# Kernel optimization log

Measured on AMD Instinct MI355X. Metric: run time of the kernel, lower is better.

The kernel has to match this reference:

```python
import jax, jax.numpy as jnp
import numpy as np

N = 50000
E = 1000000
FN = 16
FE = 8
H = 64
DH = 64
LN_EPS = 1e-5


def _layernorm(x, g, b):
    mu = jnp.mean(x, axis=-1, keepdims=True)
    var = jnp.var(x, axis=-1, keepdims=True)
    return (x - mu) * jax.lax.rsqrt(var + LN_EPS) * g + b


def setup_inputs() -> dict:
    key = jax.random.key(0)
    ks = jax.random.split(key, 24)

    def w(k, i, o):
        return jax.random.normal(k, (i, o), jnp.float32) / np.sqrt(i).astype(np.float32)

    inp = {}
    inp["x"] = jax.random.normal(ks[0], (N, FN), jnp.float32)
    inp["edge_index"] = jax.random.randint(ks[1], (2, E), 0, N, dtype=jnp.int32)
    inp["edge_attr"] = jax.random.normal(ks[2], (E, FE), jnp.float32)
    # layer 0 (in_dim = FN, residual is a Linear since FN != H)
    inp["l0_lin_w"] = w(ks[3], FE, FN); inp["l0_lin_b"] = jnp.zeros((FN,), jnp.float32)
    inp["l0_w1"] = w(ks[4], FN, H);    inp["l0_b1"] = jnp.zeros((H,), jnp.float32)
    inp["l0_w2"] = w(ks[5], H, H);     inp["l0_b2"] = jnp.zeros((H,), jnp.float32)
    inp["l0_ln_g"] = jnp.ones((H,), jnp.float32); inp["l0_ln_b"] = jnp.zeros((H,), jnp.float32)
    inp["l0_res_w"] = w(ks[6], FN, H); inp["l0_res_b"] = jnp.zeros((H,), jnp.float32)
    # layers 1, 2 (in_dim = H, residual = identity)
    for li, base in ((1, 7), (2, 11)):
        inp[f"l{li}_lin_w"] = w(ks[base], FE, H);   inp[f"l{li}_lin_b"] = jnp.zeros((H,), jnp.float32)
        inp[f"l{li}_w1"] = w(ks[base + 1], H, H);   inp[f"l{li}_b1"] = jnp.zeros((H,), jnp.float32)
        inp[f"l{li}_w2"] = w(ks[base + 2], H, H);   inp[f"l{li}_b2"] = jnp.zeros((H,), jnp.float32)
        inp[f"l{li}_ln_g"] = jnp.ones((H,), jnp.float32)
        inp[f"l{li}_ln_b"] = jnp.zeros((H,), jnp.float32)
    D_IN = 4 * H + FE
    inp["dec_w1"] = w(ks[20], D_IN, DH);    inp["dec_b1"] = jnp.zeros((DH,), jnp.float32)
    inp["dec_w2"] = w(ks[21], DH, DH // 2); inp["dec_b2"] = jnp.zeros((DH // 2,), jnp.float32)
    inp["dec_w3"] = w(ks[22], DH // 2, 1);  inp["dec_b3"] = jnp.zeros((1,), jnp.float32)
    return inp


def _block(x, src, dst, edge_attr, lin_w, lin_b, w1, b1, w2, b2, ln_g, ln_b, res):
    # GINEConv: message = ReLU(x_src + Lin(edge_attr)); sum-aggregate at dst; eps=0
    msg = jax.nn.relu(x[src] + edge_attr @ lin_w + lin_b)      # (E, D_in)
    aggr = jax.ops.segment_sum(msg, dst, num_segments=N)       # (N, D_in)
    h = jax.nn.relu((x + aggr) @ w1 + b1) @ w2 + b2            # GIN nn MLP -> (N, H)
    h = jax.nn.relu(h)                                         # dropout inactive (eval)
    return _layernorm(h + res, ln_g, ln_b)


def reference(x, edge_index, edge_attr,
              l0_lin_w, l0_lin_b, l0_w1, l0_b1, l0_w2, l0_b2, l0_ln_g, l0_ln_b, l0_res_w, l0_res_b,
              l1_lin_w, l1_lin_b, l1_w1, l1_b1, l1_w2, l1_b2, l1_ln_g, l1_ln_b,
              l2_lin_w, l2_lin_b, l2_w1, l2_b1, l2_w2, l2_b2, l2_ln_g, l2_ln_b,
              dec_w1, dec_b1, dec_w2, dec_b2, dec_w3, dec_b3):
    src, dst = edge_index[0], edge_index[1]
    h = _block(x, src, dst, edge_attr, l0_lin_w, l0_lin_b, l0_w1, l0_b1, l0_w2, l0_b2,
               l0_ln_g, l0_ln_b, x @ l0_res_w + l0_res_b)
    h = _block(h, src, dst, edge_attr, l1_lin_w, l1_lin_b, l1_w1, l1_b1, l1_w2, l1_b2,
               l1_ln_g, l1_ln_b, h)
    h = _block(h, src, dst, edge_attr, l2_lin_w, l2_lin_b, l2_w1, l2_b1, l2_w2, l2_b2,
               l2_ln_g, l2_ln_b, h)
    hs, hd = h[src], h[dst]                                    # (E, H) each
    z = jnp.concatenate([hs, hd, jnp.abs(hs - hd), hs * hd, edge_attr], axis=-1)  # (E, 4H+FE)
    z = jax.nn.relu(z @ dec_w1 + dec_b1)
    z = jax.nn.relu(z @ dec_w2 + dec_b2)
    return (z @ dec_w3 + dec_b3)[:, 0]                         # (E,)
```

## Files before the change

### kernel.cpp

```cpp
#include <hip/hip_runtime.h>

#define NN 50000
#define NE 1000000

constexpr float LN_EPS = 1e-5f;

typedef short bf16x8 __attribute__((ext_vector_type(8)));
typedef float f32x4 __attribute__((ext_vector_type(4)));
typedef uint uvec4 __attribute__((ext_vector_type(4)));
typedef uint uvec2 __attribute__((ext_vector_type(2)));

__device__ inline uint cvtpk(float a, float b) {
  uint r;
  asm("v_cvt_pk_bf16_f32 %0, %1, %2" : "=v"(r) : "v"(a), "v"(b));
  return r;
}
__device__ inline ushort cvt1(float a) {
  uint r;
  asm("v_cvt_pk_bf16_f32 %0, %1, %1" : "=v"(r) : "v"(a));
  return (ushort)r;
}
__device__ inline float bflo(uint u) { union { uint x; float f; } v; v.x = u << 16; return v.f; }
__device__ inline float bfhi(uint u) { union { uint x; float f; } v; v.x = u & 0xffff0000u; return v.f; }

__global__ __launch_bounds__(256) void hist_kernel(const int* __restrict__ ei,
                                                   int* __restrict__ cnt) {
  int e = blockIdx.x * 256 + threadIdx.x;
  if (e < NE) atomicAdd(&cnt[ei[NE + e]], 1);
}

__global__ __launch_bounds__(256) void scan1_kernel(const int* __restrict__ cnt,
                                                    int* __restrict__ off,
                                                    int* __restrict__ bsum) {
  __shared__ int sh[256];
  int t = threadIdx.x;
  int idx = blockIdx.x * 256 + t;
  int v = (idx < NN) ? cnt[idx] : 0;
  sh[t] = v;
  __syncthreads();
  for (int o = 1; o < 256; o <<= 1) {
    int xv = (t >= o) ? sh[t - o] : 0;
    __syncthreads();
    sh[t] += xv;
    __syncthreads();
  }
  if (idx <= NN) off[idx] = sh[t] - v;
  if (t == 255) bsum[blockIdx.x] = sh[255];
}

__global__ __launch_bounds__(256) void scan2_kernel(int* __restrict__ bsum, int nb) {
  __shared__ int sh[256];
  int t = threadIdx.x;
  int v = (t < nb) ? bsum[t] : 0;
  sh[t] = v;
  __syncthreads();
  for (int o = 1; o < 256; o <<= 1) {
    int xv = (t >= o) ? sh[t - o] : 0;
    __syncthreads();
    sh[t] += xv;
    __syncthreads();
  }
  if (t < nb) bsum[t] = sh[t] - v;
}

__global__ __launch_bounds__(256) void scan3_kernel(int* __restrict__ off,
                                                    const int* __restrict__ bsum,
                                                    int* __restrict__ cnt) {
  int idx = blockIdx.x * 256 + threadIdx.x;
  if (idx <= NN) off[idx] += bsum[blockIdx.x];
  if (idx < NN) cnt[idx] = 0;
}

__global__ __launch_bounds__(256) void scatter_kernel(
    const int* __restrict__ ei, const float* __restrict__ ea,
    const int* __restrict__ off, int* __restrict__ cur,
    int* __restrict__ ipos, int* __restrict__ srcp, int* __restrict__ dstp,
    ushort* __restrict__ eapb) {
  int e = blockIdx.x * 256 + threadIdx.x;
  if (e < NE) {
    int d = ei[NE + e];
    int s = ei[e];
    int p = off[d] + atomicAdd(&cur[d], 1);
    ipos[e] = p;
    srcp[p] = s;
    dstp[p] = d;
    const float* eaf = ea + (size_t)e * 8;
    f32x4 e0 = *(const f32x4*)(eaf);
    f32x4 e1 = *(const f32x4*)(eaf + 4);
    uvec4 u;
    u.x = cvtpk(e0.x, e0.y);
    u.y = cvtpk(e0.z, e0.w);
    u.z = cvtpk(e1.x, e1.y);
    u.w = cvtpk(e1.z, e1.w);
    __builtin_nontemporal_store(u, (uvec4*)(eapb + (size_t)p * 8));
  }
}

__global__ __launch_bounds__(256) void unperm_kernel(const float* __restrict__ tmp,
                                                     const int* __restrict__ ipos,
                                                     float* __restrict__ out) {
  int e = blockIdx.x * 256 + threadIdx.x;
  if (e < NE) out[e] = tmp[ipos[e]];
}

__global__ __launch_bounds__(256) void aggr0_kernel(
    const float* __restrict__ x, float* __restrict__ tout16,
    const ushort* __restrict__ eapb, const int* __restrict__ srcp,
    const int* __restrict__ off,
    const float* __restrict__ lw, const float* __restrict__ lb) {
  int n = blockIdx.x * 4 + (threadIdx.x >> 6);
  int j = threadIdx.x & 63;
  int d = j & 15, slot = j >> 4;
  int start = off[n], end = off[n + 1];
  float lwv[8];
#pragma unroll
  for (int i = 0; i < 8; i++) lwv[i] = lw[i * 16 + d];
  float lbv = lb[d];
  float acc = 0.f;
  for (int base = start; base < end; base += 64) {
    int idx = base + j;
    int sl = (idx < end) ? srcp[idx] : 0;
    int c = min(end - base, 64);
    for (int i0 = 0; i0 < c; i0 += 4) {
      int i = i0 + slot;
      bool valid = i < c;
      int ii = i & 63;
      int s = __shfl(sl, ii);
      int pp = min(base + i0 + slot, NE - 1);
      float ev = bflo((uint)eapb[(size_t)pp * 8 + (d & 7)]);
      float xs = x[(size_t)s * 16 + d];
      float m = lbv + xs;
#pragma unroll
      for (int q = 0; q < 8; q++) m = fmaf(__shfl(ev, slot * 16 + q), lwv[q], m);
      m = fmaxf(m, 0.f);
      acc += valid ? m : 0.f;
    }
  }
  acc += __shfl_xor(acc, 16);
  acc += __shfl_xor(acc, 32);
  if (slot == 0) tout16[(size_t)n * 16 + d] = acc;
}

__device__ inline float edge8_msg(const ushort* __restrict__ hinb, int s, int j,
                                  uint ulo, uint uhi, uint vlo, uint vhi,
                                  const float* lwv, float lbv) {
  float hc = bflo((uint)hinb[(size_t)s * 64 + j]);
  float m = lbv + hc;
  m = fmaf(bflo(ulo), lwv[0], m);
  m = fmaf(bfhi(ulo), lwv[1], m);
  m = fmaf(bflo(uhi), lwv[2], m);
  m = fmaf(bfhi(uhi), lwv[3], m);
  m = fmaf(bflo(vlo), lwv[4], m);
  m = fmaf(bfhi(vlo), lwv[5], m);
  m = fmaf(bflo(vhi), lwv[6], m);
  m = fmaf(bfhi(vhi), lwv[7], m);
  return fmaxf(m, 0.f);
}

__global__ __launch_bounds__(256) void aggr_kernel(
    const ushort* __restrict__ hinb, float* __restrict__ tout,
    const ushort* __restrict__ eapb, const int* __restrict__ srcp,
    const int* __restrict__ off,
    const float* __restrict__ lw, const float* __restrict__ lb) {
  int n = blockIdx.x * 4 + (threadIdx.x >> 6);
  int j = threadIdx.x & 63;
  int start = __builtin_amdgcn_readfirstlane(off[n]);
  int end = __builtin_amdgcn_readfirstlane(off[n + 1]);
  float lwv[8];
#pragma unroll
  for (int i = 0; i < 8; i++) lwv[i] = lw[i * 64 + j];
  float lbv = lb[j];
  float acc = 0.f;
  int p = start;
  for (; p + 8 <= end; p += 8) {
    const uvec4* ip = (const uvec4*)(srcp + p);
    uvec4 I0 = __builtin_nontemporal_load(ip + 0);
    uvec4 I1 = __builtin_nontemporal_load(ip + 1);
    int s0 = __builtin_amdgcn_readfirstlane((int)I0.x);
    int s1 = __builtin_amdgcn_readfirstlane((int)I0.y);
    int s2 = __builtin_amdgcn_readfirstlane((int)I0.z);
    int s3 = __builtin_amdgcn_readfirstlane((int)I0.w);
    int s4 = __builtin_amdgcn_readfirstlane((int)I1.x);
    int s5 = __builtin_amdgcn_readfirstlane((int)I1.y);
    int s6 = __builtin_amdgcn_readfirstlane((int)I1.z);
    int s7 = __builtin_amdgcn_readfirstlane((int)I1.w);
    const uvec4* ep = (const uvec4*)(eapb + (size_t)p * 8);
    uint ua[8][4];
#pragma unroll
    for (int i = 0; i < 8; i++) {
      uvec4 E = __builtin_nontemporal_load(ep + i);
      ua[i][0] = __builtin_amdgcn_readfirstlane(E.x);
      ua[i][1] = __builtin_amdgcn_readfirstlane(E.y);
      ua[i][2] = __builtin_amdgcn_readfirstlane(E.z);
      ua[i][3] = __builtin_amdgcn_readfirstlane(E.w);
    }
    acc += edge8_msg(hinb, s0, j, ua[0][0], ua[0][1], ua[0][2], ua[0][3], lwv, lbv);
    acc += edge8_msg(hinb, s1, j, ua[1][0], ua[1][1], ua[1][2], ua[1][3], lwv, lbv);
    acc += edge8_msg(hinb, s2, j, ua[2][0], ua[2][1], ua[2][2], ua[2][3], lwv, lbv);
    acc += edge8_msg(hinb, s3, j, ua[3][0], ua[3][1], ua[3][2], ua[3][3], lwv, lbv);
    acc += edge8_msg(hinb, s4, j, ua[4][0], ua[4][1], ua[4][2], ua[4][3], lwv, lbv);
    acc += edge8_msg(hinb, s5, j, ua[5][0], ua[5][1], ua[5][2], ua[5][3], lwv, lbv);
    acc += edge8_msg(hinb, s6, j, ua[6][0], ua[6][1], ua[6][2], ua[6][3], lwv, lbv);
    acc += edge8_msg(hinb, s7, j, ua[7][0], ua[7][1], ua[7][2], ua[7][3], lwv, lbv);
  }
  for (; p < end; p++) {
    int s = __builtin_amdgcn_readfirstlane(srcp[p]);
    uvec4 E = __builtin_nontemporal_load((const uvec4*)(eapb + (size_t)p * 8));
    uint e0 = __builtin_amdgcn_readfirstlane(E.x);
    uint e1 = __builtin_amdgcn_readfirstlane(E.y);
    uint e2 = __builtin_amdgcn_readfirstlane(E.z);
    uint e3 = __builtin_amdgcn_readfirstlane(E.w);
    acc += edge8_msg(hinb, s, j, e0, e1, e2, e3, lwv, lbv);
  }
  tout[(size_t)n * 64 + j] = acc;
}

__global__ __launch_bounds__(256) void prep_kernel(
    const float* __restrict__ w1, const float* __restrict__ w2,
    ushort* __restrict__ w1f, ushort* __restrict__ w2f) {
  int t = blockIdx.x * 256 + threadIdx.x;
  if (t < 18432) {
    int j = t & 7, lane = (t >> 3) & 63, f = t >> 9;
    int k = (f >> 2) * 32 + ((lane >> 4) * 8) + j;
    int n = (f & 3) * 16 + (lane & 15);
    float v = (k < 264) ? w1[k * 64 + n] : 0.f;
    w1f[t] = cvt1(v);
  } else {
    int t2 = t - 18432;
    int j = t2 & 7, lane = (t2 >> 3) & 63, f = t2 >> 9;
    int k = (f >> 1) * 32 + ((lane >> 4) * 8) + j;
    int n = (f & 1) * 16 + (lane & 15);
    w2f[t2] = cvt1(w2[k * 32 + n]);
  }
}

__global__ __launch_bounds__(256) void prep_mlpw(
    const float* __restrict__ w1a, const float* __restrict__ w2a,
    const float* __restrict__ w1b, const float* __restrict__ w2b,
    ushort* __restrict__ out) {
  int t = blockIdx.x * 256 + threadIdx.x;
  int layer = t >> 13, wsel = (t >> 12) & 1, idx = t & 4095;
  const float* w = layer ? (wsel ? w2b : w1b) : (wsel ? w2a : w1a);
  int j = idx & 7, lane = (idx >> 3) & 63, f = idx >> 9;
  int k = (f >> 2) * 32 + ((lane >> 4) * 8) + j;
  int n = (f & 3) * 16 + (lane & 15);
  float v = w[k * 64 + n];
  ushort h = cvt1(v);
  float r = v - bflo((uint)h);
  ushort lo = cvt1(r);
  int base = layer * 16384 + wsel * 8192;
  out[base + idx] = h;
  out[base + 4096 + idx] = lo;
}

__global__ __launch_bounds__(256) void prep_mlp0(
    const float* __restrict__ w1, const float* __restrict__ w2,
    const float* __restrict__ rw, ushort* __restrict__ out) {
  int t = blockIdx.x * 256 + threadIdx.x;
  if (t < 4096) {
    int which = t >> 11, idx = t & 2047;
    int j = idx & 7, lane = (idx >> 3) & 63, f = idx >> 9;
    int k = ((lane >> 4) * 8) + j;
    int n = f * 16 + (lane & 15);
    float v;
    if (which == 0) v = (k < 16) ? w1[k * 64 + n] : 0.f;
    else            v = (k >= 16) ? rw[(k - 16) * 64 + n] : 0.f;
    ushort h = cvt1(v);
    float r = v - bflo((uint)h);
    int base = which * 4096;
    out[base + idx] = h;
    out[base + 2048 + idx] = cvt1(r);
  } else {
    int idx = t - 4096;
    int j = idx & 7, lane = (idx >> 3) & 63, f = idx >> 9;
    int k = (f >> 2) * 32 + ((lane >> 4) * 8) + j;
    int n = (f & 3) * 16 + (lane & 15);
    float v = w2[k * 64 + n];
    ushort h = cvt1(v);
    float r = v - bflo((uint)h);
    out[8192 + idx] = h;
    out[12288 + idx] = cvt1(r);
  }
}

#define YS2 68

__global__ __launch_bounds__(128) void mlp_kernel(
    const float* __restrict__ tacc, const float* __restrict__ hinf,
    float* __restrict__ houtf, ushort* __restrict__ houtbf,
    const ushort* __restrict__ wf,
    const float* __restrict__ b1, const float* __restrict__ b2,
    const float* __restrict__ lng, const float* __restrict__ lnb) {
  __shared__ float ybuf[2][32 * YS2];
  const int w = threadIdx.x >> 6, l = threadIdx.x & 63;
  const int sub = l & 15, quad = l >> 4;
  const int wid = blockIdx.x * 2 + w;
  const int r0 = wid * 32;
  if (r0 >= NN) return;
  float* Y = ybuf[w];

  const bf16x8* w1h = (const bf16x8*)wf;
  const bf16x8* w1l = (const bf16x8*)(wf + 4096);
  const bf16x8* w2h = (const bf16x8*)(wf + 8192);
  const bf16x8* w2l = (const bf16x8*)(wf + 12288);

  union UF { uvec4 u; bf16x8 v; };

  bf16x8 Ahi[2][2], Alo[2][2];
#pragma unroll
  for (int m = 0; m < 2; m++) {
    int row = min(r0 + m * 16 + sub, NN - 1);
    const float* pt = tacc + (size_t)row * 64 + quad * 8;
    const float* ph = hinf + (size_t)row * 64 + quad * 8;
#pragma unroll
    for (int ks = 0; ks < 2; ks++) {
      f32x4 t0 = *(const f32x4*)(pt + ks * 32);
      f32x4 t1 = *(const f32x4*)(pt + ks * 32 + 4);
      f32x4 h0 = *(const f32x4*)(ph + ks * 32);
      f32x4 h1 = *(const f32x4*)(ph + ks * 32 + 4);
      t0 += h0;
      t1 += h1;
      UF uh, ul;
      uh.u.x = cvtpk(t0.x, t0.y);
      uh.u.y = cvtpk(t0.z, t0.w);
      uh.u.z = cvtpk(t1.x, t1.y);
      uh.u.w = cvtpk(t1.z, t1.w);
      ul.u.x = cvtpk(t0.x - bflo(uh.u.x), t0.y - bfhi(uh.u.x));
      ul.u.y = cvtpk(t0.z - bflo(uh.u.y), t0.w - bfhi(uh.u.y));
      ul.u.z = cvtpk(t1.x - bflo(uh.u.z), t1.y - bfhi(uh.u.z));
      ul.u.w = cvtpk(t1.z - bflo(uh.u.w), t1.w - bfhi(uh.u.w));
      Ahi[m][ks] = uh.v;
      Alo[m][ks] = ul.v;
    }
  }

  f32x4 c1[2][4];
#pragma unroll
  for (int m = 0; m < 2; m++)
#pragma unroll
    for (int nb = 0; nb < 4; nb++) c1[m][nb] = (f32x4){0.f, 0.f, 0.f, 0.f};
#pragma unroll
  for (int nb = 0; nb < 4; nb++) {
#pragma unroll
    for (int ks = 0; ks < 2; ks++) {
      bf16x8 bh = w1h[(ks * 4 + nb) * 64 + l];
      bf16x8 bl = w1l[(ks * 4 + nb) * 64 + l];
      c1[0][nb] = __builtin_amdgcn_mfma_f32_16x16x32_bf16(Ahi[0][ks], bh, c1[0][nb], 0, 0, 0);
      c1[1][nb] = __builtin_amdgcn_mfma_f32_16x16x32_bf16(Ahi[1][ks], bh, c1[1][nb], 0, 0, 0);
      c1[0][nb] = __builtin_amdgcn_mfma_f32_16x16x32_bf16(Alo[0][ks], bh, c1[0][nb], 0, 0, 0);
      c1[1][nb] = __builtin_amdgcn_mfma_f32_16x16x32_bf16(Alo[1][ks], bh, c1[1][nb], 0, 0, 0);
      c1[0][nb] = __builtin_amdgcn_mfma_f32_16x16x32_bf16(Ahi[0][ks], bl, c1[0][nb], 0, 0, 0);
      c1[1][nb] = __builtin_amdgcn_mfma_f32_16x16x32_bf16(Ahi[1][ks], bl, c1[1][nb], 0, 0, 0);
    }
  }

  float b1v[4];
#pragma unroll
  for (int nb = 0; nb < 4; nb++) b1v[nb] = b1[nb * 16 + sub];
#pragma unroll
  for (int m = 0; m < 2; m++)
#pragma unroll
    for (int nb = 0; nb < 4; nb++)
#pragma unroll
      for (int r = 0; r < 4; r++)
        Y[(m * 16 + quad * 4 + r) * YS2 + nb * 16 + sub] =
            fmaxf(c1[m][nb][r] + b1v[nb], 0.f);

  bf16x8 Qhi[2][2], Qlo[2][2];
#pragma unroll
  for (int m = 0; m < 2; m++) {
#pragma unroll
    for (int ks = 0; ks < 2; ks++) {
      const float* py = &Y[(m * 16 + sub) * YS2 + ks * 32 + quad * 8];
      f32x4 q0 = *(const f32x4*)py;
      f32x4 q1 = *(const f32x4*)(py + 4);
      UF uh, ul;
      uh.u.x = cvtpk(q0.x, q0.y);
      uh.u.y = cvtpk(q0.z, q0.w);
      uh.u.z = cvtpk(q1.x, q1.y);
      uh.u.w = cvtpk(q1.z, q1.w);
      ul.u.x = cvtpk(q0.x - bflo(uh.u.x), q0.y - bfhi(uh.u.x));
      ul.u.y = cvtpk(q0.z - bflo(uh.u.y), q0.w - bfhi(uh.u.y));
      ul.u.z = cvtpk(q1.x - bflo(uh.u.z), q1.y - bfhi(uh.u.z));
      ul.u.w = cvtpk(q1.z - bflo(uh.u.w), q1.w - bfhi(uh.u.w));
      Qhi[m][ks] = uh.v;
      Qlo[m][ks] = ul.v;
    }
  }

  f32x4 c2[2][4];
#pragma unroll
  for (int m = 0; m < 2; m++)
#pragma unroll
    for (int nb = 0; nb < 4; nb++) c2[m][nb] = (f32x4){0.f, 0.f, 0.f, 0.f};
#pragma unroll
  for (int nb = 0; nb < 4; nb++) {
#pragma unroll
    for (int ks = 0; ks < 2; ks++) {
      bf16x8 bh = w2h[(ks * 4 + nb) * 64 + l];
      bf16x8 bl = w2l[(ks * 4 + nb) * 64 + l];
      c2[0][nb] = __builtin_amdgcn_mfma_f32_16x16x32_bf16(Qhi[0][ks], bh, c2[0][nb], 0, 0, 0);
      c2[1][nb] = __builtin_amdgcn_mfma_f32_16x16x32_bf16(Qhi[1][ks], bh, c2[1][nb], 0, 0, 0);
      c2[0][nb] = __builtin_amdgcn_mfma_f32_16x16x32_bf16(Qlo[0][ks], bh, c2[0][nb], 0, 0, 0);
      c2[1][nb] = __builtin_amdgcn_mfma_f32_16x16x32_bf16(Qlo[1][ks], bh, c2[1][nb], 0, 0, 0);
      c2[0][nb] = __builtin_amdgcn_mfma_f32_16x16x32_bf16(Qhi[0][ks], bl, c2[0][nb], 0, 0, 0);
      c2[1][nb] = __builtin_amdgcn_mfma_f32_16x16x32_bf16(Qhi[1][ks], bl, c2[1][nb], 0, 0, 0);
    }
  }

  float b2v[4], lngv[4], lnbv[4];
#pragma unroll
  for (int nb = 0; nb < 4; nb++) {
    b2v[nb] = b2[nb * 16 + sub];
    lngv[nb] = lng[nb * 16 + sub];
    lnbv[nb] = lnb[nb * 16 + sub];
  }
#pragma unroll
  for (int m = 0; m < 2; m++) {
#pragma unroll
    for (int r = 0; r < 4; r++) {
      int node = r0 + m * 16 + quad * 4 + r;
      int nc = min(node, NN - 1);
      float vp[4];
      float s = 0.f;
#pragma unroll
      for (int nb = 0; nb < 4; nb++) {
        vp[nb] = fmaxf(c2[m][nb][r] + b2v[nb], 0.f) +
                 hinf[(size_t)nc * 64 + nb * 16 + sub];
        s += vp[nb];
      }
      s += __shfl_xor(s, 1);
      s += __shfl_xor(s, 2);
      s += __shfl_xor(s, 4);
      s += __shfl_xor(s, 8);
      float mu = s * (1.f / 64.f);
      float vv = 0.f;
      float dv[4];
#pragma unroll
      for (int nb = 0; nb < 4; nb++) {
        dv[nb] = vp[nb] - mu;
        vv += dv[nb] * dv[nb];
      }
      vv += __shfl_xor(vv, 1);
      vv += __shfl_xor(vv, 2);
      vv += __shfl_xor(vv, 4);
      vv += __shfl_xor(vv, 8);
      float rstd = rsqrtf(vv * (1.f / 64.f) + LN_EPS);
      if (node < NN) {
#pragma unroll
        for (int nb = 0; nb < 4; nb++) {
          float o = dv[nb] * rstd * lngv[nb] + lnbv[nb];
          if (houtf) houtf[(size_t)node * 64 + nb * 16 + sub] = o;
          houtbf[(size_t)node * 64 + nb * 16 + sub] = cvt1(o);
        }
      }
    }
  }
}

__global__ __launch_bounds__(128) void mlp0_kernel(
    const float* __restrict__ x, const float* __restrict__ tacc16,
    float* __restrict__ houtf, ushort* __restrict__ houtbf,
    const ushort* __restrict__ wf,
    const float* __restrict__ b1, const float* __restrict__ b2,
    const float* __restrict__ rb,
    const float* __restrict__ lng, const float* __restrict__ lnb) {
  __shared__ float ybuf[2][32 * YS2];
  const int w = threadIdx.x >> 6, l = threadIdx.x & 63;
  const int sub = l & 15, quad = l >> 4;
  const int wid = blockIdx.x * 2 + w;
  const int r0 = wid * 32;
  if (r0 >= NN) return;
  float* Y = ybuf[w];

  const bf16x8* B1h = (const bf16x8*)wf;
  const bf16x8* B1l = (const bf16x8*)(wf + 2048);
  const bf16x8* B2h = (const bf16x8*)(wf + 4096);
  const bf16x8* B2l = (const bf16x8*)(wf + 6144);
  const bf16x8* W2h = (const bf16x8*)(wf + 8192);
  const bf16x8* W2l = (const bf16x8*)(wf + 12288);

  union UF { uvec4 u; bf16x8 v; };

  bf16x8 Ahi[2], Alo[2];
#pragma unroll
  for (int m = 0; m < 2; m++) {
    int row = min(r0 + m * 16 + sub, NN - 1);
    const float* px = x + (size_t)row * 16 + (quad & 1) * 8;
    f32x4 v0 = *(const f32x4*)px;
    f32x4 v1 = *(const f32x4*)(px + 4);
    if (quad < 2) {
      const float* pt = tacc16 + (size_t)row * 16 + (quad & 1) * 8;
      v0 += *(const f32x4*)pt;
      v1 += *(const f32x4*)(pt + 4);
    }
    UF uh, ul;
    uh.u.x = cvtpk(v0.x, v0.y);
    uh.u.y = cvtpk(v0.z, v0.w);
    uh.u.z = cvtpk(v1.x, v1.y);
    uh.u.w = cvtpk(v1.z, v1.w);
    ul.u.x = cvtpk(v0.x - bflo(uh.u.x), v0.y - bfhi(uh.u.x));
    ul.u.y = cvtpk(v0.z - bflo(uh.u.y), v0.w - bfhi(uh.u.y));
    ul.u.z = cvtpk(v1.x - bflo(uh.u.z), v1.y - bfhi(uh.u.z));
    ul.u.w = cvtpk(v1.z - bflo(uh.u.w), v1.w - bfhi(uh.u.w));
    Ahi[m] = uh.v;
    Alo[m] = ul.v;
  }

  f32x4 c1[2][4], cr[2][4];
#pragma unroll
  for (int m = 0; m < 2; m++)
#pragma unroll
    for (int nb = 0; nb < 4; nb++) {
      c1[m][nb] = (f32x4){0.f, 0.f, 0.f, 0.f};
      cr[m][nb] = (f32x4){0.f, 0.f, 0.f, 0.f};
    }
#pragma unroll
  for (int nb = 0; nb < 4; nb++) {
    bf16x8 bh = B1h[nb * 64 + l];
    bf16x8 bl = B1l[nb * 64 + l];
    c1[0][nb] = __builtin_amdgcn_mfma_f32_16x16x32_bf16(Ahi[0], bh, c1[0][nb], 0, 0, 0);
    c1[1][nb] = __builtin_amdgcn_mfma_f32_16x16x32_bf16(Ahi[1], bh, c1[1][nb], 0, 0, 0);
    c1[0][nb] = __builtin_amdgcn_mfma_f32_16x16x32_bf16(Alo[0], bh, c1[0][nb], 0, 0, 0);
    c1[1][nb] = __builtin_amdgcn_mfma_f32_16x16x32_bf16(Alo[1], bh, c1[1][nb], 0, 0, 0);
    c1[0][nb] = __builtin_amdgcn_mfma_f32_16x16x32_bf16(Ahi[0], bl, c1[0][nb], 0, 0, 0);
    c1[1][nb] = __builtin_amdgcn_mfma_f32_16x16x32_bf16(Ahi[1], bl, c1[1][nb], 0, 0, 0);
    bf16x8 rh = B2h[nb * 64 + l];
    bf16x8 rl = B2l[nb * 64 + l];
    cr[0][nb] = __builtin_amdgcn_mfma_f32_16x16x32_bf16(Ahi[0], rh, cr[0][nb], 0, 0, 0);
    cr[1][nb] = __builtin_amdgcn_mfma_f32_16x16x32_bf16(Ahi[1], rh, cr[1][nb], 0, 0, 0);
    cr[0][nb] = __builtin_amdgcn_mfma_f32_16x16x32_bf16(Alo[0], rh, cr[0][nb], 0, 0, 0);
    cr[1][nb] = __builtin_amdgcn_mfma_f32_16x16x32_bf16(Alo[1], rh, cr[1][nb], 0, 0, 0);
    cr[0][nb] = __builtin_amdgcn_mfma_f32_16x16x32_bf16(Ahi[0], rl, cr[0][nb], 0, 0, 0);
    cr[1][nb] = __builtin_amdgcn_mfma_f32_16x16x32_bf16(Ahi[1], rl, cr[1][nb], 0, 0, 0);
  }

  float b1v[4];
#pragma unroll
  for (int nb = 0; nb < 4; nb++) b1v[nb] = b1[nb * 16 + sub];
#pragma unroll
  for (int m = 0; m < 2; m++)
#pragma unroll
    for (int nb = 0; nb < 4; nb++)
#pragma unroll
      for (int r = 0; r < 4; r++)
        Y[(m * 16 + quad * 4 + r) * YS2 + nb * 16 + sub] =
            fmaxf(c1[m][nb][r] + b1v[nb], 0.f);

  bf16x8 Qhi[2][2], Qlo[2][2];
#pragma unroll
  for (int m = 0; m < 2; m++) {
#pragma unroll
    for (int ks = 0; ks < 2; ks++) {
      const float* py = &Y[(m * 16 + sub) * YS2 + ks * 32 + quad * 8];
      f32x4 q0 = *(const f32x4*)py;
      f32x4 q1 = *(const f32x4*)(py + 4);
      UF uh, ul;
      uh.u.x = cvtpk(q0.x, q0.y);
      uh.u.y = cvtpk(q0.z, q0.w);
      uh.u.z = cvtpk(q1.x, q1.y);
      uh.u.w = cvtpk(q1.z, q1.w);
      ul.u.x = cvtpk(q0.x - bflo(uh.u.x), q0.y - bfhi(uh.u.x));
      ul.u.y = cvtpk(q0.z - bflo(uh.u.y), q0.w - bfhi(uh.u.y));
      ul.u.z = cvtpk(q1.x - bflo(uh.u.z), q1.y - bfhi(uh.u.z));
      ul.u.w = cvtpk(q1.z - bflo(uh.u.w), q1.w - bfhi(uh.u.w));
      Qhi[m][ks] = uh.v;
      Qlo[m][ks] = ul.v;
    }
  }

  f32x4 c2[2][4];
#pragma unroll
  for (int m = 0; m < 2; m++)
#pragma unroll
    for (int nb = 0; nb < 4; nb++) c2[m][nb] = (f32x4){0.f, 0.f, 0.f, 0.f};
#pragma unroll
  for (int nb = 0; nb < 4; nb++) {
#pragma unroll
    for (int ks = 0; ks < 2; ks++) {
      bf16x8 bh = W2h[(ks * 4 + nb) * 64 + l];
      bf16x8 bl = W2l[(ks * 4 + nb) * 64 + l];
      c2[0][nb] = __builtin_amdgcn_mfma_f32_16x16x32_bf16(Qhi[0][ks], bh, c2[0][nb], 0, 0, 0);
      c2[1][nb] = __builtin_amdgcn_mfma_f32_16x16x32_bf16(Qhi[1][ks], bh, c2[1][nb], 0, 0, 0);
      c2[0][nb] = __builtin_amdgcn_mfma_f32_16x16x32_bf16(Qlo[0][ks], bh, c2[0][nb], 0, 0, 0);
      c2[1][nb] = __builtin_amdgcn_mfma_f32_16x16x32_bf16(Qlo[1][ks], bh, c2[1][nb], 0, 0, 0);
      c2[0][nb] = __builtin_amdgcn_mfma_f32_16x16x32_bf16(Qhi[0][ks], bl, c2[0][nb], 0, 0, 0);
      c2[1][nb] = __builtin_amdgcn_mfma_f32_16x16x32_bf16(Qhi[1][ks], bl, c2[1][nb], 0, 0, 0);
    }
  }

  float b2v[4], rbv[4], lngv[4], lnbv[4];
#pragma unroll
  for (int nb = 0; nb < 4; nb++) {
    b2v[nb] = b2[nb * 16 + sub];
    rbv[nb] = rb[nb * 16 + sub];
    lngv[nb] = lng[nb * 16 + sub];
    lnbv[nb] = lnb[nb * 16 + sub];
  }
#pragma unroll
  for (int m = 0; m < 2; m++) {
#pragma unroll
    for (int r = 0; r < 4; r++) {
      int node = r0 + m * 16 + quad * 4 + r;
      float vp[4];
      float s = 0.f;
#pragma unroll
      for (int nb = 0; nb < 4; nb++) {
        vp[nb] = fmaxf(c2[m][nb][r] + b2v[nb], 0.f) + cr[m][nb][r] + rbv[nb];
        s += vp[nb];
      }
      s += __shfl_xor(s, 1);
      s += __shfl_xor(s, 2);
      s += __shfl_xor(s, 4);
      s += __shfl_xor(s, 8);
      float mu = s * (1.f / 64.f);
      float vv = 0.f;
      float dv[4];
#pragma unroll
      for (int nb = 0; nb < 4; nb++) {
        dv[nb] = vp[nb] - mu;
        vv += dv[nb] * dv[nb];
      }
      vv += __shfl_xor(vv, 1);
      vv += __shfl_xor(vv, 2);
      vv += __shfl_xor(vv, 4);
      vv += __shfl_xor(vv, 8);
      float rstd = rsqrtf(vv * (1.f / 64.f) + LN_EPS);
      if (node < NN) {
#pragma unroll
        for (int nb = 0; nb < 4; nb++) {
          float o = dv[nb] * rstd * lngv[nb] + lnbv[nb];
          houtf[(size_t)node * 64 + nb * 16 + sub] = o;
          houtbf[(size_t)node * 64 + nb * 16 + sub] = cvt1(o);
        }
      }
    }
  }
}

#define YS 72
#define NBLK 15625
#define BPX 1954

__device__ inline void absmul(bf16x8 a, bf16x8 b, bf16x8& dd, bf16x8& pp) {
  union U { bf16x8 v; uvec4 u; } ua, ub, ud, up;
  ua.v = a; ub.v = b;
#pragma unroll
  for (int i = 0; i < 4; i++) {
    float a0 = bflo(ua.u[i]), a1 = bfhi(ua.u[i]);
    float b0 = bflo(ub.u[i]), b1 = bfhi(ub.u[i]);
    ud.u[i] = cvtpk(fabsf(a0 - b0), fabsf(a1 - b1));
    up.u[i] = cvtpk(a0 * b0, a1 * b1);
  }
  dd = ud.v; pp = up.v;
}

__global__ __launch_bounds__(128, 4) void decoder_kernel(
    const ushort* __restrict__ hb,
    const int* __restrict__ srcp, const int* __restrict__ dstp,
    const ushort* __restrict__ eapb,
    const ushort* __restrict__ w1f, const ushort* __restrict__ w2f,
    const float* __restrict__ b1, const float* __restrict__ b2,
    const float* __restrict__ w3, const float* __restrict__ b3,
    float* __restrict__ tmp) {
  __shared__ ushort ybuf[2][32 * YS];
  const int w = threadIdx.x >> 6, l = threadIdx.x & 63;
  const int sub = l & 15, quad = l >> 4;
  int bb = (blockIdx.x & 7) * BPX + (blockIdx.x >> 3);
  if (bb >= NBLK) return;
  const int g = bb * 2 + w;
  ushort* Y = ybuf[w];

  int s32 = __builtin_nontemporal_load(&srcp[g * 32 + (l & 31)]);
  int d32 = __builtin_nontemporal_load(&dstp[g * 32 + (l & 31)]);

  bf16x8 alo[2], ahi[2], blo[2], bhi[2];
#pragma unroll
  for (int m = 0; m < 2; m++) {
    int sA = __shfl(s32, m * 16 + sub);
    int dA = __shfl(d32, m * 16 + sub);
    const ushort* pa = hb + (size_t)sA * 64 + quad * 8;
    const ushort* pb = hb + (size_t)dA * 64 + quad * 8;
    alo[m] = *(const bf16x8*)pa;
    ahi[m] = *(const bf16x8*)(pa + 32);
    blo[m] = *(const bf16x8*)pb;
    bhi[m] = *(const bf16x8*)(pb + 32);
  }
  bf16x8 eaf0 = (bf16x8){0, 0, 0, 0, 0, 0, 0, 0};
  bf16x8 eaf1 = (bf16x8){0, 0, 0, 0, 0, 0, 0, 0};
  if (quad == 0) {
    eaf0 = *(const bf16x8*)&eapb[((size_t)g * 32 + sub) * 8];
    eaf1 = *(const bf16x8*)&eapb[((size_t)g * 32 + 16 + sub) * 8];
  }

  float b1v[4];
#pragma unroll
  for (int t = 0; t < 4; t++) b1v[t] = b1[t * 16 + sub];
  float b2v0 = b2[sub], b2v1 = b2[16 + sub];
  float w3v0 = w3[sub], w3v1 = w3[16 + sub];
  float b3v = b3[0];

  f32x4 acc[2][4];
#pragma unroll
  for (int m = 0; m < 2; m++)
#pragma unroll
    for (int t = 0; t < 4; t++) acc[m][t] = (f32x4){0.f, 0.f, 0.f, 0.f};

#define MF(sB, f0, f1)                                                        \
  {                                                                           \
    _Pragma("unroll") for (int t = 0; t < 4; t++) {                           \
      bf16x8 bfv = ((const bf16x8*)w1f)[((sB)*4 + t) * 64 + l];               \
      acc[0][t] = __builtin_amdgcn_mfma_f32_16x16x32_bf16(f0, bfv, acc[0][t], \
                                                          0, 0, 0);           \
      acc[1][t] = __builtin_amdgcn_mfma_f32_16x16x32_bf16(f1, bfv, acc[1][t], \
                                                          0, 0, 0);           \
    }                                                                         \
  }

  {
    bf16x8 dlo0, plo0, dlo1, plo1;
    absmul(alo[0], blo[0], dlo0, plo0);
    absmul(alo[1], blo[1], dlo1, plo1);
    MF(0, alo[0], alo[1]);
    MF(2, blo[0], blo[1]);
    MF(4, dlo0, dlo1);
    MF(6, plo0, plo1);
  }
  {
    bf16x8 dhi0, phi0, dhi1, phi1;
    absmul(ahi[0], bhi[0], dhi0, phi0);
    absmul(ahi[1], bhi[1], dhi1, phi1);
    MF(1, ahi[0], ahi[1]);
    MF(3, bhi[0], bhi[1]);
    MF(5, dhi0, dhi1);
    MF(7, phi0, phi1);
  }
  MF(8, eaf0, eaf1);
#undef MF

#pragma unroll
  for (int m = 0; m < 2; m++)
#pragma unroll
    for (int t = 0; t < 4; t++)
#pragma unroll
      for (int r = 0; r < 4; r++)
        Y[(m * 16 + quad * 4 + r) * YS + t * 16 + sub] =
            cvt1(fmaxf(acc[m][t][r] + b1v[t], 0.f));

  bf16x8 w2frag[4];
#pragma unroll
  for (int f = 0; f < 4; f++) w2frag[f] = ((const bf16x8*)w2f)[f * 64 + l];
  f32x4 acc2[2][2];
#pragma unroll
  for (int m = 0; m < 2; m++) {
    acc2[m][0] = (f32x4){0.f, 0.f, 0.f, 0.f};
    acc2[m][1] = (f32x4){0.f, 0.f, 0.f, 0.f};
#pragma unroll
    for (int ks = 0; ks < 2; ks++) {
      bf16x8 ya = *(const bf16x8*)&Y[(m * 16 + sub) * YS + ks * 32 + quad * 8];
      acc2[m][0] = __builtin_amdgcn_mfma_f32_16x16x32_bf16(ya, w2frag[ks * 2 + 0],
                                                           acc2[m][0], 0, 0, 0);
      acc2[m][1] = __builtin_amdgcn_mfma_f32_16x16x32_bf16(ya, w2frag[ks * 2 + 1],
                                                           acc2[m][1], 0, 0, 0);
    }
  }
#pragma unroll
  for (int m = 0; m < 2; m++)
#pragma unroll
    for (int r = 0; r < 4; r++) {
      float o = fmaxf(acc2[m][0][r] + b2v0, 0.f) * w3v0 +
                fmaxf(acc2[m][1][r] + b2v1, 0.f) * w3v1;
      o += __shfl_xor(o, 1);
      o += __shfl_xor(o, 2);
      o += __shfl_xor(o, 4);
      o += __shfl_xor(o, 8);
      if (sub == 0) tmp[g * 32 + m * 16 + quad * 4 + r] = o + b3v;
    }
}

extern "C" void kernel_launch(void* const* d_in, const int* in_sizes, int n_in,
                              void* d_out, int out_size, void* d_ws, size_t ws_size,
                              hipStream_t stream) {
  const float* x = (const float*)d_in[0];
  const int* ei = (const int*)d_in[1];
  const float* ea = (const float*)d_in[2];
  const float* l0_lin_w = (const float*)d_in[3];
  const float* l0_lin_b = (const float*)d_in[4];
  const float* l0_w1 = (const float*)d_in[5];
  const float* l0_b1 = (const float*)d_in[6];
  const float* l0_w2 = (const float*)d_in[7];
  const float* l0_b2 = (const float*)d_in[8];
  const float* l0_ln_g = (const float*)d_in[9];
  const float* l0_ln_b = (const float*)d_in[10];
  const float* l0_res_w = (const float*)d_in[11];
  const float* l0_res_b = (const float*)d_in[12];
  const float* dec_w1 = (const float*)d_in[29];
  const float* dec_b1 = (const float*)d_in[30];
  const float* dec_w2 = (const float*)d_in[31];
  const float* dec_b2 = (const float*)d_in[32];
  const float* dec_w3 = (const float*)d_in[33];
  const float* dec_b3 = (const float*)d_in[34];

  float* h_a = (float*)d_ws;
  float* h_b = h_a + (size_t)NN * 64;
  ushort* hbA = (ushort*)(h_b + (size_t)NN * 64);
  ushort* hbB = hbA + (size_t)NN * 64;
  int* ipos = (int*)(hbB + (size_t)NN * 64);
  int* srcp = ipos + NE;
  int* dstp = srcp + NE;
  float* tmp = (float*)(dstp + NE);
  int* off = (int*)(tmp + NE);
  int* cnt = off + (NN + 1);
  int* bsum = cnt + NN;
  ushort* w1f = (ushort*)(bsum + 256);
  ushort* w2f = w1f + 18432;
  ushort* eapb = w2f + 2048;
  ushort* wmlp = eapb + (size_t)NE * 8;
  ushort* wmlp0 = wmlp + 32768;
  float* tacc = (float*)(wmlp0 + 16384);

  const int EB = (NE + 255) / 256;
  const int SB = (NN + 256) / 256;
  const int MB = ((NN + 31) / 32 + 1) / 2;

  hipMemsetAsync(cnt, 0, (size_t)NN * sizeof(int), stream);
  hist_kernel<<<EB, 256, 0, stream>>>(ei, cnt);
  scan1_kernel<<<SB, 256, 0, stream>>>(cnt, off, bsum);
  scan2_kernel<<<1, 256, 0, stream>>>(bsum, SB);
  scan3_kernel<<<SB, 256, 0, stream>>>(off, bsum, cnt);
  scatter_kernel<<<EB, 256, 0, stream>>>(ei, ea, off, cnt, ipos, srcp, dstp, eapb);
  prep_mlpw<<<64, 256, 0, stream>>>((const float*)d_in[15], (const float*)d_in[17],
                                    (const float*)d_in[23], (const float*)d_in[25],
                                    wmlp);
  prep_mlp0<<<32, 256, 0, stream>>>(l0_w1, l0_w2, l0_res_w, wmlp0);

  aggr0_kernel<<<NN / 4, 256, 0, stream>>>(x, tacc, eapb, srcp, off,
                                           l0_lin_w, l0_lin_b);
  mlp0_kernel<<<MB, 128, 0, stream>>>(x, tacc, h_a, hbA, wmlp0,
                                      l0_b1, l0_b2, l0_res_b, l0_ln_g, l0_ln_b);

  aggr_kernel<<<NN / 4, 256, 0, stream>>>(hbA, tacc, eapb, srcp, off,
                                          (const float*)d_in[13],
                                          (const float*)d_in[14]);
  mlp_kernel<<<MB, 128, 0, stream>>>(tacc, h_a, h_b, hbB, wmlp,
                                     (const float*)d_in[16], (const float*)d_in[18],
                                     (const float*)d_in[19], (const float*)d_in[20]);
  aggr_kernel<<<NN / 4, 256, 0, stream>>>(hbB, tacc, eapb, srcp, off,
                                          (const float*)d_in[21],
                                          (const float*)d_in[22]);
  mlp_kernel<<<MB, 128, 0, stream>>>(tacc, h_b, (float*)nullptr, hbA, wmlp + 16384,
                                     (const float*)d_in[24], (const float*)d_in[26],
                                     (const float*)d_in[27], (const float*)d_in[28]);

  prep_kernel<<<80, 256, 0, stream>>>(dec_w1, dec_w2, w1f, w2f);
  decoder_kernel<<<8 * BPX, 128, 0, stream>>>(hbA, srcp, dstp, eapb,
                                              w1f, w2f, dec_b1, dec_b2,
                                              dec_w3, dec_b3, tmp);
  unperm_kernel<<<EB, 256, 0, stream>>>(tmp, ipos, (float*)d_out);
}
```

Measured before the change: 543.8 us.

## Process two edge groups per decoder wave and use 256-thread blocks

```diff
diff --git a/kernel.cpp b/kernel.cpp
--- a/kernel.cpp
+++ b/kernel.cpp
@@ -639,8 +639,9 @@
 }
 
 #define YS 72
-#define NBLK 15625
-#define BPX 1954
+#define NGRP 31250
+#define NBLKD 3907
+#define BPXD 489
 
 __device__ inline void absmul(bf16x8 a, bf16x8 b, bf16x8& dd, bf16x8& pp) {
   union U { bf16x8 v; uvec4 u; } ua, ub, ud, up;
@@ -655,7 +656,7 @@
   dd = ud.v; pp = up.v;
 }
 
-__global__ __launch_bounds__(128, 4) void decoder_kernel(
+__global__ __launch_bounds__(256, 4) void decoder_kernel(
     const ushort* __restrict__ hb,
     const int* __restrict__ srcp, const int* __restrict__ dstp,
     const ushort* __restrict__ eapb,
@@ -663,34 +664,45 @@
     const float* __restrict__ b1, const float* __restrict__ b2,
     const float* __restrict__ w3, const float* __restrict__ b3,
     float* __restrict__ tmp) {
-  __shared__ ushort ybuf[2][32 * YS];
+  __shared__ ushort ybuf[4][32 * YS];
   const int w = threadIdx.x >> 6, l = threadIdx.x & 63;
   const int sub = l & 15, quad = l >> 4;
-  int bb = (blockIdx.x & 7) * BPX + (blockIdx.x >> 3);
-  if (bb >= NBLK) return;
-  const int g = bb * 2 + w;
+  int bb = (blockIdx.x & 7) * BPXD + (blockIdx.x >> 3);
+  if (bb >= NBLKD) return;
+  const int G = bb * 8 + w * 2;
   ushort* Y = ybuf[w];
 
-  int s32 = __builtin_nontemporal_load(&srcp[g * 32 + (l & 31)]);
-  int d32 = __builtin_nontemporal_load(&dstp[g * 32 + (l & 31)]);
-
-  bf16x8 alo[2], ahi[2], blo[2], bhi[2];
-#pragma unroll
-  for (int m = 0; m < 2; m++) {
-    int sA = __shfl(s32, m * 16 + sub);
-    int dA = __shfl(d32, m * 16 + sub);
-    const ushort* pa = hb + (size_t)sA * 64 + quad * 8;
-    const ushort* pb = hb + (size_t)dA * 64 + quad * 8;
-    alo[m] = *(const bf16x8*)pa;
-    ahi[m] = *(const bf16x8*)(pa + 32);
-    blo[m] = *(const bf16x8*)pb;
-    bhi[m] = *(const bf16x8*)(pb + 32);
-  }
-  bf16x8 eaf0 = (bf16x8){0, 0, 0, 0, 0, 0, 0, 0};
-  bf16x8 eaf1 = (bf16x8){0, 0, 0, 0, 0, 0, 0, 0};
+  int gg = min(G + (l >> 5), NGRP - 1);
+  int s64 = __builtin_nontemporal_load(&srcp[gg * 32 + (l & 31)]);
+  int d64 = __builtin_nontemporal_load(&dstp[gg * 32 + (l & 31)]);
+
+  bf16x8 alo[2][2], ahi[2][2], blo[2][2], bhi[2][2];
+#pragma unroll
+  for (int q = 0; q < 2; q++)
+#pragma unroll
+    for (int m = 0; m < 2; m++) {
+      int sA = __shfl(s64, q * 32 + m * 16 + sub);
+      int dA = __shfl(d64, q * 32 + m * 16 + sub);
+      const ushort* pa = hb + (size_t)sA * 64 + quad * 8;
+      const ushort* pb = hb + (size_t)dA * 64 + quad * 8;
+      alo[q][m] = *(const bf16x8*)pa;
+      ahi[q][m] = *(const bf16x8*)(pa + 32);
+      blo[q][m] = *(const bf16x8*)pb;
+      bhi[q][m] = *(const bf16x8*)(pb + 32);
+    }
+  bf16x8 eaf[2][2];
+#pragma unroll
+  for (int q = 0; q < 2; q++) {
+    eaf[q][0] = (bf16x8){0, 0, 0, 0, 0, 0, 0, 0};
+    eaf[q][1] = (bf16x8){0, 0, 0, 0, 0, 0, 0, 0};
+  }
   if (quad == 0) {
-    eaf0 = *(const bf16x8*)&eapb[((size_t)g * 32 + sub) * 8];
-    eaf1 = *(const bf16x8*)&eapb[((size_t)g * 32 + 16 + sub) * 8];
+#pragma unroll
+    for (int q = 0; q < 2; q++) {
+      size_t gc = (size_t)min(G + q, NGRP - 1);
+      eaf[q][0] = *(const bf16x8*)&eapb[(gc * 32 + sub) * 8];
+      eaf[q][1] = *(const bf16x8*)&eapb[(gc * 32 + 16 + sub) * 8];
+    }
   }
 
   float b1v[4];
@@ -700,82 +712,88 @@
   float w3v0 = w3[sub], w3v1 = w3[16 + sub];
   float b3v = b3[0];
 
-  f32x4 acc[2][4];
-#pragma unroll
-  for (int m = 0; m < 2; m++)
-#pragma unroll
-    for (int t = 0; t < 4; t++) acc[m][t] = (f32x4){0.f, 0.f, 0.f, 0.f};
-
-#define MF(sB, f0, f1)                                                        \
-  {                                                                           \
-    _Pragma("unroll") for (int t = 0; t < 4; t++) {                           \
-      bf16x8 bfv = ((const bf16x8*)w1f)[((sB)*4 + t) * 64 + l];               \
-      acc[0][t] = __builtin_amdgcn_mfma_f32_16x16x32_bf16(f0, bfv, acc[0][t], \
-                                                          0, 0, 0);           \
-      acc[1][t] = __builtin_amdgcn_mfma_f32_16x16x32_bf16(f1, bfv, acc[1][t], \
-                                                          0, 0, 0);           \
-    }                                                                         \
-  }
-
-  {
-    bf16x8 dlo0, plo0, dlo1, plo1;
-    absmul(alo[0], blo[0], dlo0, plo0);
-    absmul(alo[1], blo[1], dlo1, plo1);
-    MF(0, alo[0], alo[1]);
-    MF(2, blo[0], blo[1]);
-    MF(4, dlo0, dlo1);
-    MF(6, plo0, plo1);
-  }
-  {
-    bf16x8 dhi0, phi0, dhi1, phi1;
-    absmul(ahi[0], bhi[0], dhi0, phi0);
-    absmul(ahi[1], bhi[1], dhi1, phi1);
-    MF(1, ahi[0], ahi[1]);
-    MF(3, bhi[0], bhi[1]);
-    MF(5, dhi0, dhi1);
-    MF(7, phi0, phi1);
-  }
-  MF(8, eaf0, eaf1);
+#pragma unroll
+  for (int q = 0; q < 2; q++) {
+    const int g = G + q;
+
+    f32x4 acc[2][4];
+#pragma unroll
+    for (int m = 0; m < 2; m++)
+#pragma unroll
+      for (int t = 0; t < 4; t++) acc[m][t] = (f32x4){0.f, 0.f, 0.f, 0.f};
+
+#define MF(sB, f0, f1)                                                          \
+    {                                                                           \
+      _Pragma("unroll") for (int t = 0; t < 4; t++) {                           \
+        bf16x8 bfv = ((const bf16x8*)w1f)[((sB)*4 + t) * 64 + l];               \
+        acc[0][t] = __builtin_amdgcn_mfma_f32_16x16x32_bf16(f0, bfv, acc[0][t], \
+                                                            0, 0, 0);           \
+        acc[1][t] = __builtin_amdgcn_mfma_f32_16x16x32_bf16(f1, bfv, acc[1][t], \
+                                                            0, 0, 0);           \
+      }                                                                         \
+    }
+
+    {
+      bf16x8 dlo0, plo0, dlo1, plo1;
+      absmul(alo[q][0], blo[q][0], dlo0, plo0);
+      absmul(alo[q][1], blo[q][1], dlo1, plo1);
+      MF(0, alo[q][0], alo[q][1]);
+      MF(2, blo[q][0], blo[q][1]);
+      MF(4, dlo0, dlo1);
+      MF(6, plo0, plo1);
+    }
+    {
+      bf16x8 dhi0, phi0, dhi1, phi1;
+      absmul(ahi[q][0], bhi[q][0], dhi0, phi0);
+      absmul(ahi[q][1], bhi[q][1], dhi1, phi1);
+      MF(1, ahi[q][0], ahi[q][1]);
+      MF(3, bhi[q][0], bhi[q][1]);
+      MF(5, dhi0, dhi1);
+      MF(7, phi0, phi1);
+    }
+    MF(8, eaf[q][0], eaf[q][1]);
 #undef MF
 
 #pragma unroll
-  for (int m = 0; m < 2; m++)
-#pragma unroll
-    for (int t = 0; t < 4; t++)
-#pragma unroll
-      for (int r = 0; r < 4; r++)
-        Y[(m * 16 + quad * 4 + r) * YS + t * 16 + sub] =
-            cvt1(fmaxf(acc[m][t][r] + b1v[t], 0.f));
-
-  bf16x8 w2frag[4];
-#pragma unroll
-  for (int f = 0; f < 4; f++) w2frag[f] = ((const bf16x8*)w2f)[f * 64 + l];
-  f32x4 acc2[2][2];
-#pragma unroll
-  for (int m = 0; m < 2; m++) {
-    acc2[m][0] = (f32x4){0.f, 0.f, 0.f, 0.f};
-    acc2[m][1] = (f32x4){0.f, 0.f, 0.f, 0.f};
-#pragma unroll
-    for (int ks = 0; ks < 2; ks++) {
-      bf16x8 ya = *(const bf16x8*)&Y[(m * 16 + sub) * YS + ks * 32 + quad * 8];
-      acc2[m][0] = __builtin_amdgcn_mfma_f32_16x16x32_bf16(ya, w2frag[ks * 2 + 0],
-                                                           acc2[m][0], 0, 0, 0);
-      acc2[m][1] = __builtin_amdgcn_mfma_f32_16x16x32_bf16(ya, w2frag[ks * 2 + 1],
-                                                           acc2[m][1], 0, 0, 0);
-    }
-  }
-#pragma unroll
-  for (int m = 0; m < 2; m++)
-#pragma unroll
-    for (int r = 0; r < 4; r++) {
-      float o = fmaxf(acc2[m][0][r] + b2v0, 0.f) * w3v0 +
-                fmaxf(acc2[m][1][r] + b2v1, 0.f) * w3v1;
-      o += __shfl_xor(o, 1);
-      o += __shfl_xor(o, 2);
-      o += __shfl_xor(o, 4);
-      o += __shfl_xor(o, 8);
-      if (sub == 0) tmp[g * 32 + m * 16 + quad * 4 + r] = o + b3v;
-    }
+    for (int m = 0; m < 2; m++)
+#pragma unroll
+      for (int t = 0; t < 4; t++)
+#pragma unroll
+        for (int r = 0; r < 4; r++)
+          Y[(m * 16 + quad * 4 + r) * YS + t * 16 + sub] =
+              cvt1(fmaxf(acc[m][t][r] + b1v[t], 0.f));
+
+    bf16x8 w2frag[4];
+#pragma unroll
+    for (int f = 0; f < 4; f++) w2frag[f] = ((const bf16x8*)w2f)[f * 64 + l];
+    f32x4 acc2[2][2];
+#pragma unroll
+    for (int m = 0; m < 2; m++) {
+      acc2[m][0] = (f32x4){0.f, 0.f, 0.f, 0.f};
+      acc2[m][1] = (f32x4){0.f, 0.f, 0.f, 0.f};
+#pragma unroll
+      for (int ks = 0; ks < 2; ks++) {
+        bf16x8 ya = *(const bf16x8*)&Y[(m * 16 + sub) * YS + ks * 32 + quad * 8];
+        acc2[m][0] = __builtin_amdgcn_mfma_f32_16x16x32_bf16(ya, w2frag[ks * 2 + 0],
+                                                             acc2[m][0], 0, 0, 0);
+        acc2[m][1] = __builtin_amdgcn_mfma_f32_16x16x32_bf16(ya, w2frag[ks * 2 + 1],
+                                                             acc2[m][1], 0, 0, 0);
+      }
+    }
+#pragma unroll
+    for (int m = 0; m < 2; m++)
+#pragma unroll
+      for (int r = 0; r < 4; r++) {
+        float o = fmaxf(acc2[m][0][r] + b2v0, 0.f) * w3v0 +
+                  fmaxf(acc2[m][1][r] + b2v1, 0.f) * w3v1;
+        o += __shfl_xor(o, 1);
+        o += __shfl_xor(o, 2);
+        o += __shfl_xor(o, 4);
+        o += __shfl_xor(o, 8);
+        if (sub == 0 && g < NGRP)
+          tmp[g * 32 + m * 16 + quad * 4 + r] = o + b3v;
+      }
+  }
 }
 
 extern "C" void kernel_launch(void* const* d_in, const int* in_sizes, int n_in,
@@ -853,8 +871,8 @@
                                      (const float*)d_in[27], (const float*)d_in[28]);
 
   prep_kernel<<<80, 256, 0, stream>>>(dec_w1, dec_w2, w1f, w2f);
-  decoder_kernel<<<8 * BPX, 128, 0, stream>>>(hbA, srcp, dstp, eapb,
-                                              w1f, w2f, dec_b1, dec_b2,
-                                              dec_w3, dec_b3, tmp);
+  decoder_kernel<<<8 * BPXD, 256, 0, stream>>>(hbA, srcp, dstp, eapb,
+                                               w1f, w2f, dec_b1, dec_b2,
+                                               dec_w3, dec_b3, tmp);
   unperm_kernel<<<EB, 256, 0, stream>>>(tmp, ipos, (float*)d_out);
 }
```

After: 592.6 us. 1.09x slower.
